# Performance work log

Measured on AMD Instinct MI355X. Metric: run time of the kernel, lower is better.

## Reference

```python
import jax, jax.numpy as jnp
import numpy as np

RATIO = 0.5


def _fps_indices(points, m):
    """Farthest point sampling indices. points: [B,N,3] -> idx [B,m] (int32).
    Deterministic start at index 0 per batch (torch_geometric fps with a fixed start).
    """
    pts = jax.lax.stop_gradient(points)  # index selection is non-differentiable
    B, N, _ = pts.shape
    idx0 = jnp.zeros((B,), dtype=jnp.int32)
    mind0 = jnp.full((B, N), 1e10, dtype=pts.dtype)  # running min sq-distance to selected set

    def step(carry, _):
        mind, last = carry
        last_pt = jnp.take_along_axis(pts, last[:, None, None], axis=1)  # [B,1,3]
        d = jnp.sum((pts - last_pt) ** 2, axis=-1)                       # [B,N]
        mind = jnp.minimum(mind, d)
        nxt = jnp.argmax(mind, axis=1).astype(jnp.int32)                 # farthest point
        return (mind, nxt), nxt

    _, rest = jax.lax.scan(step, (mind0, idx0), None, length=m - 1)      # [m-1, B]
    return jnp.concatenate([idx0[None, :], rest], axis=0).T              # [B, m]


def setup_inputs() -> dict:
    key = jax.random.key(0)
    k1, k2 = jax.random.split(key)
    points = jax.random.normal(k1, (8, 8192, 3), dtype=jnp.float32)
    features = jax.random.normal(k2, (8, 8192, 256), dtype=jnp.float32)
    return {"points": points, "features": features}


def reference(points, features):
    B, N, _ = points.shape
    m = int(np.ceil(RATIO * N))
    idx = _fps_indices(points, m)                                        # [B, m]
    dp = jnp.take_along_axis(points, idx[:, :, None], axis=1)            # [B, m, 3]
    df = jnp.take_along_axis(features, idx[:, :, None], axis=1)          # [B, m, C]
    return dp, df
```

## Files before the change

### kernel.cpp

```cpp
#include <hip/hip_runtime.h>


typedef float v2f __attribute__((ext_vector_type(2)));

#define BATCH 8
#define NPTS  8192
#define MSEL  4096
#define NFEAT 256
#define BLOCK 1024

__device__ __forceinline__ double sqd(double x) {
    double r;
    asm("v_mul_f64 %0, %1, %1" : "=v"(r) : "v"(x));
    return r;
}

__device__ __forceinline__ unsigned wave_umax(unsigned v) {
    unsigned t;
    t = (unsigned)__builtin_amdgcn_update_dpp(0, (int)v, 0x111, 0xf, 0xf, false); v = v > t ? v : t;
    t = (unsigned)__builtin_amdgcn_update_dpp(0, (int)v, 0x112, 0xf, 0xf, false); v = v > t ? v : t;
    t = (unsigned)__builtin_amdgcn_update_dpp(0, (int)v, 0x114, 0xf, 0xf, false); v = v > t ? v : t;
    t = (unsigned)__builtin_amdgcn_update_dpp(0, (int)v, 0x118, 0xf, 0xf, false); v = v > t ? v : t;
    t = (unsigned)__builtin_amdgcn_update_dpp(0, (int)v, 0x142, 0xf, 0xf, false); v = v > t ? v : t;
    t = (unsigned)__builtin_amdgcn_update_dpp(0, (int)v, 0x143, 0xf, 0xf, false); v = v > t ? v : t;
    return (unsigned)__builtin_amdgcn_readlane((int)v, 63);
}

__launch_bounds__(BLOCK, 1)
__global__ void fps_kernel(const float* __restrict__ pts,
                           float* __restrict__ dp,
                           int* __restrict__ idx_out)
{
    __shared__ float s_pts[NPTS * 3];
    __shared__ unsigned long long s_bmax[2];
    __shared__ int s_widx[2];

    const int b   = blockIdx.x;
    const int tid = threadIdx.x;
    const float* p = pts + (size_t)b * NPTS * 3;

    for (int i = tid; i < NPTS * 3; i += BLOCK) s_pts[i] = p[i];
    if (tid == 0) {
        s_bmax[0] = 0ull;        s_bmax[1] = 0ull;
        s_widx[0] = 0x7fffffff;  s_widx[1] = 0x7fffffff;
    }

#define DECLP(P, J0, J1) \
    v2f pxp##P = { p[(tid + J0 * 1024) * 3 + 0], p[(tid + J1 * 1024) * 3 + 0] }; \
    v2f pyp##P = { p[(tid + J0 * 1024) * 3 + 1], p[(tid + J1 * 1024) * 3 + 1] }; \
    v2f pzp##P = { p[(tid + J0 * 1024) * 3 + 2], p[(tid + J1 * 1024) * 3 + 2] };
    DECLP(0, 0, 1) DECLP(1, 2, 3) DECLP(2, 4, 5) DECLP(3, 6, 7)
#undef DECLP
    double mind0 = 1e10, mind1 = 1e10, mind2 = 1e10, mind3 = 1e10;
    double mind4 = 1e10, mind5 = 1e10, mind6 = 1e10, mind7 = 1e10;
    float  mfm0 = 1.0001e10f, mfm1 = 1.0001e10f, mfm2 = 1.0001e10f, mfm3 = 1.0001e10f;
    float  mfm4 = 1.0001e10f, mfm5 = 1.0001e10f, mfm6 = 1.0001e10f, mfm7 = 1.0001e10f;

    float cx = p[0], cy = p[1], cz = p[2];
    if (tid == 0) {
        dp[(size_t)b * MSEL * 3 + 0] = cx;
        dp[(size_t)b * MSEL * 3 + 1] = cy;
        dp[(size_t)b * MSEL * 3 + 2] = cz;
        idx_out[b * MSEL + 0] = 0;
    }

    const int lane = tid & 63;
    double tbv   = 0.0;
    bool   dirty = true;

    __syncthreads();

    for (int k = 1; k < MSEL; ++k) {
        const double cxd = (double)cx, cyd = (double)cy, czd = (double)cz;
        const v2f cx2 = {cx, cx}, cy2 = {cy, cy}, cz2 = {cz, cz};

#define EX64(PX, PY, PZ, J) { \
        const double ddx = (double)(PX) - cxd; \
        const double ddy = (double)(PY) - cyd; \
        const double ddz = (double)(PZ) - czd; \
        const double dd  = (sqd(ddx) + sqd(ddy)) + sqd(ddz); \
        if (dd < mind##J) { mind##J = dd; mfm##J = (float)dd * 1.0001f; dirty = true; } }
#define UPDP(P, J0, J1) { \
        const v2f dx = pxp##P - cx2, dy = pyp##P - cy2, dz = pzp##P - cz2; \
        const v2f d  = dx * dx + dy * dy + dz * dz; \
        if (d.x < mfm##J0) EX64(pxp##P.x, pyp##P.x, pzp##P.x, J0) \
        if (d.y < mfm##J1) EX64(pxp##P.y, pyp##P.y, pzp##P.y, J1) }
        UPDP(0, 0, 1) UPDP(1, 2, 3) UPDP(2, 4, 5) UPDP(3, 6, 7)
#undef UPDP
#undef EX64

        if (dirty) {
            const double a0 = fmax(mind0, mind1), a1 = fmax(mind2, mind3);
            const double a2 = fmax(mind4, mind5), a3 = fmax(mind6, mind7);
            tbv = fmax(fmax(a0, a1), fmax(a2, a3));
            dirty = false;
        }

        const unsigned long long tb = (unsigned long long)__double_as_longlong(tbv);
        const unsigned thi  = (unsigned)(tb >> 32);
        const unsigned hmax = wave_umax(thi);
        const unsigned lpart = (thi == hmax) ? (unsigned)tb : 0u;
        const unsigned lmax = wave_umax(lpart);
        if (lane == 0)
            atomicMax(&s_bmax[k & 1],
                      ((unsigned long long)hmax << 32) | (unsigned long long)lmax);
        __syncthreads();

        const unsigned long long bmaxbits = s_bmax[k & 1];
        if (tid == 0) {
            s_bmax[(k + 1) & 1] = 0ull;
            s_widx[(k + 1) & 1] = 0x7fffffff;
        }

        if ((unsigned long long)__double_as_longlong(tbv) == bmaxbits) {
            int n = 0x7fffffff;
            if (mind7 == tbv) n = tid + 7 * 1024;
            if (mind6 == tbv) n = tid + 6 * 1024;
            if (mind5 == tbv) n = tid + 5 * 1024;
            if (mind4 == tbv) n = tid + 4 * 1024;
            if (mind3 == tbv) n = tid + 3 * 1024;
            if (mind2 == tbv) n = tid + 2 * 1024;
            if (mind1 == tbv) n = tid + 1 * 1024;
            if (mind0 == tbv) n = tid;
            atomicMin(&s_widx[k & 1], n);
        }
        __syncthreads();

        const int   widx = s_widx[k & 1];
        const float wx = s_pts[widx * 3 + 0];
        const float wy = s_pts[widx * 3 + 1];
        const float wz = s_pts[widx * 3 + 2];
        if (tid == 0) {
            idx_out[b * MSEL + k] = widx;
            float* o = dp + ((size_t)b * MSEL + k) * 3;
            o[0] = wx; o[1] = wy; o[2] = wz;
        }
        cx = wx; cy = wy; cz = wz;
    }
}

__global__ void gather_kernel(const float* __restrict__ feats,
                              const int* __restrict__ idx,
                              float* __restrict__ df)
{
    const int row  = blockIdx.x * 4 + (threadIdx.x >> 6);
    const int lane = threadIdx.x & 63;
    const int b    = row >> 12;
    const int src  = idx[row];
    const float4* s = (const float4*)(feats + ((size_t)b * NPTS + src) * NFEAT);
    float4*       d = (float4*)(df + (size_t)row * NFEAT);
    d[lane] = s[lane];
}

extern "C" void kernel_launch(void* const* d_in, const int* in_sizes, int n_in,
                              void* d_out, int out_size, void* d_ws, size_t ws_size,
                              hipStream_t stream)
{
    const float* points   = (const float*)d_in[0];
    const float* features = (const float*)d_in[1];
    float* out = (float*)d_out;
    float* dp  = out;
    float* df  = out + (size_t)BATCH * MSEL * 3;
    int*   idx_ws = (int*)d_ws;

    fps_kernel<<<BATCH, BLOCK, 0, stream>>>(points, dp, idx_ws);
    gather_kernel<<<(BATCH * MSEL) / 4, 256, 0, stream>>>(features, idx_ws, df);
}
```

Measured before the change: 4.239 ms.

## Replace two-barrier atomic argmax with per-wave pairs and single-barrier DPP reduction

Each iteration now computes the wave-level max distance and its smallest winning index inside the wave, writes one (value, index) pair per wave to shared memory, and then every wave reduces the 16 pairs lexicographically with DPP. This drops the second __syncthreads and the shared-memory atomics per FPS step. The wave reduction is also skipped when no lane in the wave changed its min-distance, with the cached pair reused. The cost is more DPP work per step, since all waves redundantly run the 16-entry reduction.

```diff
diff --git a/kernel.cpp b/kernel.cpp
--- a/kernel.cpp
+++ b/kernel.cpp
@@ -26,24 +26,41 @@
     return (unsigned)__builtin_amdgcn_readlane((int)v, 63);
 }
 
+__device__ __forceinline__ unsigned wave_umin(unsigned v) {
+    unsigned t;
+    t = (unsigned)__builtin_amdgcn_update_dpp(-1, (int)v, 0x111, 0xf, 0xf, false); v = v < t ? v : t;
+    t = (unsigned)__builtin_amdgcn_update_dpp(-1, (int)v, 0x112, 0xf, 0xf, false); v = v < t ? v : t;
+    t = (unsigned)__builtin_amdgcn_update_dpp(-1, (int)v, 0x114, 0xf, 0xf, false); v = v < t ? v : t;
+    t = (unsigned)__builtin_amdgcn_update_dpp(-1, (int)v, 0x118, 0xf, 0xf, false); v = v < t ? v : t;
+    t = (unsigned)__builtin_amdgcn_update_dpp(-1, (int)v, 0x142, 0xf, 0xf, false); v = v < t ? v : t;
+    t = (unsigned)__builtin_amdgcn_update_dpp(-1, (int)v, 0x143, 0xf, 0xf, false); v = v < t ? v : t;
+    return (unsigned)__builtin_amdgcn_readlane((int)v, 63);
+}
+
+template <int CTRL>
+__device__ __forceinline__ void lex_stage(unsigned& hi, unsigned& lo, unsigned& idx) {
+    const unsigned ohi  = (unsigned)__builtin_amdgcn_update_dpp(0,  (int)hi,  CTRL, 0xf, 0xf, false);
+    const unsigned olo  = (unsigned)__builtin_amdgcn_update_dpp(0,  (int)lo,  CTRL, 0xf, 0xf, false);
+    const unsigned oidx = (unsigned)__builtin_amdgcn_update_dpp(-1, (int)idx, CTRL, 0xf, 0xf, false);
+    const bool take = (ohi > hi) || (ohi == hi && ((olo > lo) || (olo == lo && oidx < idx)));
+    hi  = take ? ohi  : hi;
+    lo  = take ? olo  : lo;
+    idx = take ? oidx : idx;
+}
+
 __launch_bounds__(BLOCK, 1)
 __global__ void fps_kernel(const float* __restrict__ pts,
                            float* __restrict__ dp,
                            int* __restrict__ idx_out)
 {
     __shared__ float s_pts[NPTS * 3];
-    __shared__ unsigned long long s_bmax[2];
-    __shared__ int s_widx[2];
+    __shared__ ulonglong2 s_pair[2][16];
 
     const int b   = blockIdx.x;
     const int tid = threadIdx.x;
     const float* p = pts + (size_t)b * NPTS * 3;
 
     for (int i = tid; i < NPTS * 3; i += BLOCK) s_pts[i] = p[i];
-    if (tid == 0) {
-        s_bmax[0] = 0ull;        s_bmax[1] = 0ull;
-        s_widx[0] = 0x7fffffff;  s_widx[1] = 0x7fffffff;
-    }
 
 #define DECLP(P, J0, J1) \
     v2f pxp##P = { p[(tid + J0 * 1024) * 3 + 0], p[(tid + J1 * 1024) * 3 + 0] }; \
@@ -65,21 +82,24 @@
     }
 
     const int lane = tid & 63;
-    double tbv   = 0.0;
-    bool   dirty = true;
+    const int wid  = tid >> 6;
+
+    unsigned long long wbits = 0ull;
+    unsigned           widxw = 0xffffffffu;
 
     __syncthreads();
 
     for (int k = 1; k < MSEL; ++k) {
         const double cxd = (double)cx, cyd = (double)cy, czd = (double)cz;
         const v2f cx2 = {cx, cx}, cy2 = {cy, cy}, cz2 = {cz, cz};
+        bool upd = false;
 
 #define EX64(PX, PY, PZ, J) { \
         const double ddx = (double)(PX) - cxd; \
         const double ddy = (double)(PY) - cyd; \
         const double ddz = (double)(PZ) - czd; \
         const double dd  = (sqd(ddx) + sqd(ddy)) + sqd(ddz); \
-        if (dd < mind##J) { mind##J = dd; mfm##J = (float)dd * 1.0001f; dirty = true; } }
+        if (dd < mind##J) { mind##J = dd; mfm##J = (float)dd * 1.0001f; upd = true; } }
 #define UPDP(P, J0, J1) { \
         const v2f dx = pxp##P - cx2, dy = pyp##P - cy2, dz = pzp##P - cz2; \
         const v2f d  = dx * dx + dy * dy + dz * dz; \
@@ -89,44 +109,44 @@
 #undef UPDP
 #undef EX64
 
-        if (dirty) {
+        if (__ballot(upd) != 0ull) {
             const double a0 = fmax(mind0, mind1), a1 = fmax(mind2, mind3);
             const double a2 = fmax(mind4, mind5), a3 = fmax(mind6, mind7);
-            tbv = fmax(fmax(a0, a1), fmax(a2, a3));
-            dirty = false;
+            const double tbv = fmax(fmax(a0, a1), fmax(a2, a3));
+
+            const unsigned long long tb = (unsigned long long)__double_as_longlong(tbv);
+            const unsigned thi  = (unsigned)(tb >> 32);
+            const unsigned hmax = wave_umax(thi);
+            const unsigned lmax = wave_umax((thi == hmax) ? (unsigned)tb : 0u);
+            wbits = ((unsigned long long)hmax << 32) | (unsigned long long)lmax;
+
+            unsigned n = 0xffffffffu;
+            if ((unsigned long long)__double_as_longlong(tbv) == wbits) {
+                if (mind7 == tbv) n = (unsigned)(tid + 7 * 1024);
+                if (mind6 == tbv) n = (unsigned)(tid + 6 * 1024);
+                if (mind5 == tbv) n = (unsigned)(tid + 5 * 1024);
+                if (mind4 == tbv) n = (unsigned)(tid + 4 * 1024);
+                if (mind3 == tbv) n = (unsigned)(tid + 3 * 1024);
+                if (mind2 == tbv) n = (unsigned)(tid + 2 * 1024);
+                if (mind1 == tbv) n = (unsigned)(tid + 1 * 1024);
+                if (mind0 == tbv) n = (unsigned)tid;
+            }
+            widxw = wave_umin(n);
         }
-
-        const unsigned long long tb = (unsigned long long)__double_as_longlong(tbv);
-        const unsigned thi  = (unsigned)(tb >> 32);
-        const unsigned hmax = wave_umax(thi);
-        const unsigned lpart = (thi == hmax) ? (unsigned)tb : 0u;
-        const unsigned lmax = wave_umax(lpart);
         if (lane == 0)
-            atomicMax(&s_bmax[k & 1],
-                      ((unsigned long long)hmax << 32) | (unsigned long long)lmax);
+            s_pair[k & 1][wid] = (ulonglong2){wbits, (unsigned long long)widxw};
         __syncthreads();
 
-        const unsigned long long bmaxbits = s_bmax[k & 1];
-        if (tid == 0) {
-            s_bmax[(k + 1) & 1] = 0ull;
-            s_widx[(k + 1) & 1] = 0x7fffffff;
-        }
+        const ulonglong2 e = s_pair[k & 1][lane & 15];
+        unsigned hi  = (unsigned)(e.x >> 32);
+        unsigned lo  = (unsigned)e.x;
+        unsigned idx = (unsigned)e.y;
+        lex_stage<0x111>(hi, lo, idx);
+        lex_stage<0x112>(hi, lo, idx);
+        lex_stage<0x114>(hi, lo, idx);
+        lex_stage<0x118>(hi, lo, idx);
+        const int widx = __builtin_amdgcn_readlane((int)idx, 15);
 
-        if ((unsigned long long)__double_as_longlong(tbv) == bmaxbits) {
-            int n = 0x7fffffff;
-            if (mind7 == tbv) n = tid + 7 * 1024;
-            if (mind6 == tbv) n = tid + 6 * 1024;
-            if (mind5 == tbv) n = tid + 5 * 1024;
-            if (mind4 == tbv) n = tid + 4 * 1024;
-            if (mind3 == tbv) n = tid + 3 * 1024;
-            if (mind2 == tbv) n = tid + 2 * 1024;
-            if (mind1 == tbv) n = tid + 1 * 1024;
-            if (mind0 == tbv) n = tid;
-            atomicMin(&s_widx[k & 1], n);
-        }
-        __syncthreads();
-
-        const int   widx = s_widx[k & 1];
         const float wx = s_pts[widx * 3 + 0];
         const float wy = s_pts[widx * 3 + 1];
         const float wz = s_pts[widx * 3 + 2];
```

Result: slower. 5.024 ms (+18.5%).
